# Optimization experiments

Hardware: AMD Instinct MI355X
Metric: run time of the kernel (lower is better)

The kernel has to match this reference:

```python
import jax, jax.numpy as jnp
import numpy as np
import math

IMG_COUNT = 5      # total_length = id_length + 1
NUM_TOKENS = 576   # (768//32)**2, the is_1024_resolution branch
CHANNELS = 1280
N_SEL = 288        # sa32 * NUM_TOKENS
HEADS = 20


def setup_inputs() -> dict:
    key = jax.random.key(0)
    ks = jax.random.split(key, 7)
    hidden_states = jax.random.normal(ks[0], (2 * IMG_COUNT, NUM_TOKENS, CHANNELS), dtype=jnp.float32)
    scale = 0.02
    Wq = jax.random.normal(ks[1], (CHANNELS, CHANNELS), dtype=jnp.float32) * scale
    Wk = jax.random.normal(ks[2], (CHANNELS, CHANNELS), dtype=jnp.float32) * scale
    Wv = jax.random.normal(ks[3], (CHANNELS, CHANNELS), dtype=jnp.float32) * scale
    Wo = jax.random.normal(ks[4], (CHANNELS, CHANNELS), dtype=jnp.float32) * scale
    bo = jnp.zeros((CHANNELS,), dtype=jnp.float32)
    # per-image random spatial token subsets (cal_attn_indice_xl_effcient_memory)
    indices = jax.random.randint(ks[5], (IMG_COUNT, N_SEL), 0, NUM_TOKENS, dtype=jnp.int64)
    return {"hidden_states": hidden_states, "Wq": Wq, "Wk": Wk, "Wv": Wv,
            "Wo": Wo, "bo": bo, "indices": indices, "heads": HEADS}


def _sdpa_block(q_in, kv_in, Wq, Wk, Wv, Wo, bo, heads):
    """Faithful __call2__: linear q/k/v, multi-head SDPA, output projection."""
    B, Tq, C = q_in.shape
    Tk = kv_in.shape[1]
    hd = C // heads
    q = (q_in @ Wq.T).reshape(B, Tq, heads, hd).transpose(0, 2, 1, 3)   # [B,H,Tq,hd]
    k = (kv_in @ Wk.T).reshape(B, Tk, heads, hd).transpose(0, 2, 1, 3)  # [B,H,Tk,hd]
    v = (kv_in @ Wv.T).reshape(B, Tk, heads, hd).transpose(0, 2, 1, 3)
    scale = 1.0 / math.sqrt(hd)
    scores = jnp.einsum('bhqd,bhkd->bhqk', q, k) * scale
    probs = jax.nn.softmax(scores, axis=-1)
    o = jnp.einsum('bhqk,bhkd->bhqd', probs, v)
    o = o.transpose(0, 2, 1, 3).reshape(B, Tq, C)
    return o @ Wo.T + bo


def reference(hidden_states, Wq, Wk, Wv, Wo, bo, indices, heads):
    B, T, C = hidden_states.shape
    P = indices.shape[0]          # img_count
    hs = hidden_states.reshape(2, P, T, C)
    # gathered[p] = hs[:, p, indices[p], :] -> [2, P, n_sel, C]
    gathered = hs[:, jnp.arange(P)[:, None], indices, :]
    outs = []
    for i in range(P):            # small fixed loop over images (structurally distinct KV banks)
        cur = hs[:, i]            # [2, T, C]
        others = jnp.concatenate([gathered[:, p] for p in range(P) if p != i], axis=1)
        enc = jnp.concatenate([others, cur], axis=1)  # [2, (P-1)*n_sel + T, C]
        outs.append(_sdpa_block(cur, enc, Wq, Wk, Wv, Wo, bo, heads))
    return jnp.stack(outs, axis=1).reshape(B, T, C)
```

## Files before the change

### kernel.cpp

```cpp
#include <hip/hip_runtime.h>

typedef __bf16 bf16_t;
typedef __attribute__((ext_vector_type(4))) __bf16 bf16x4;
typedef __attribute__((ext_vector_type(8))) __bf16 bf16x8;
typedef __attribute__((ext_vector_type(4))) float f32x4;

#define MFMA_BF16(a, b, c) __builtin_amdgcn_mfma_f32_16x16x32_bf16((a), (b), (c), 0, 0, 0)

namespace {

constexpr int PIMG  = 5;
constexpr int TTOK  = 576;
constexpr int CCH   = 1280;
constexpr int NSEL  = 288;
constexpr int NH    = 20;
constexpr int ROWS  = 2 * PIMG * TTOK;
constexpr int TKEYS = 4 * NSEL + TTOK;
constexpr int KT_TILES = TKEYS / 64;
constexpr size_t NXE = (size_t)ROWS * CCH;
constexpr size_t NWE = (size_t)CCH * CCH;

__device__ __forceinline__ bf16x8 cvt8(const float* p) {
  const float4 f0 = *(const float4*)p;
  const float4 f1 = *(const float4*)(p + 4);
  bf16x8 r;
  r[0] = (bf16_t)f0.x; r[1] = (bf16_t)f0.y; r[2] = (bf16_t)f0.z; r[3] = (bf16_t)f0.w;
  r[4] = (bf16_t)f1.x; r[5] = (bf16_t)f1.y; r[6] = (bf16_t)f1.z; r[7] = (bf16_t)f1.w;
  return r;
}

__global__ __launch_bounds__(256) void cvt_kernel(
    const float* __restrict__ X, const float* __restrict__ W0, const float* __restrict__ W1,
    const float* __restrict__ W2, const float* __restrict__ W3,
    bf16_t* __restrict__ Xb, bf16_t* __restrict__ Wb0, bf16_t* __restrict__ Wb1,
    bf16_t* __restrict__ Wb2, bf16_t* __restrict__ Wb3) {
  const int y = blockIdx.y;
  const float* src = y == 0 ? X : (y == 1 ? W0 : (y == 2 ? W1 : (y == 3 ? W2 : W3)));
  bf16_t* dst = y == 0 ? Xb : (y == 1 ? Wb0 : (y == 2 ? Wb1 : (y == 3 ? Wb2 : Wb3)));
  const size_t n = y == 0 ? NXE : NWE;
  const size_t idx = ((size_t)blockIdx.x * 256 + threadIdx.x) * 8;
  if (idx < n) *(bf16x8*)&dst[idx] = cvt8(&src[idx]);
}

template <bool BIAS, typename CT>
__device__ __forceinline__ void gemm_nt_body(const bf16_t* __restrict__ A,
                                             const bf16_t* __restrict__ B,
                                             const float* __restrict__ bias,
                                             CT* __restrict__ C,
                                             int bm, int bn, float scale) {
  constexpr int LDT = 72;
  __shared__ bf16_t As[128 * LDT];
  __shared__ bf16_t Bs[128 * LDT];

  const int tid  = threadIdx.x;
  const int lane = tid & 63;
  const int wave = tid >> 6;
  const int quad = lane >> 4;
  const int l16  = lane & 15;
  const int wr   = (wave >> 1) * 64;
  const int wc   = (wave & 1) * 64;
  const int m0   = bm * 128;
  const int n0   = bn * 128;
  const int srow = tid >> 3;
  const int scol = (tid & 7) * 8;

  bf16x8 pa[4], pb[4];
  auto loadAB = [&](int k0) {
#pragma unroll
    for (int p = 0; p < 4; ++p) {
      pa[p] = *(const bf16x8*)&A[(size_t)(m0 + srow + 32 * p) * CCH + k0 + scol];
      pb[p] = *(const bf16x8*)&B[(size_t)(n0 + srow + 32 * p) * CCH + k0 + scol];
    }
  };
  loadAB(0);

  f32x4 acc[4][4];
#pragma unroll
  for (int i = 0; i < 4; ++i)
#pragma unroll
    for (int j = 0; j < 4; ++j) acc[i][j] = (f32x4){0.f, 0.f, 0.f, 0.f};

  for (int it = 0; it < CCH / 64; ++it) {
#pragma unroll
    for (int p = 0; p < 4; ++p) {
      *(bf16x8*)&As[(srow + 32 * p) * LDT + scol] = pa[p];
      *(bf16x8*)&Bs[(srow + 32 * p) * LDT + scol] = pb[p];
    }
    __syncthreads();
    if (it < CCH / 64 - 1) loadAB((it + 1) * 64);
#pragma unroll
    for (int ks = 0; ks < 2; ++ks) {
      bf16x8 af[4], bfr[4];
#pragma unroll
      for (int i = 0; i < 4; ++i)
        af[i] = *(const bf16x8*)&As[(wr + 16 * i + l16) * LDT + ks * 32 + quad * 8];
#pragma unroll
      for (int j = 0; j < 4; ++j)
        bfr[j] = *(const bf16x8*)&Bs[(wc + 16 * j + l16) * LDT + ks * 32 + quad * 8];
#pragma unroll
      for (int i = 0; i < 4; ++i)
#pragma unroll
        for (int j = 0; j < 4; ++j)
          acc[i][j] = MFMA_BF16(af[i], bfr[j], acc[i][j]);
    }
    if (it < CCH / 64 - 1) __syncthreads();
  }

#pragma unroll
  for (int j = 0; j < 4; ++j) {
    const int col = n0 + wc + 16 * j + l16;
    const float bv = BIAS ? bias[col] : 0.f;
#pragma unroll
    for (int i = 0; i < 4; ++i) {
#pragma unroll
      for (int r = 0; r < 4; ++r) {
        const int row = m0 + wr + 16 * i + quad * 4 + r;
        const float val = acc[i][j][r] * scale + bv;
        if constexpr (sizeof(CT) == 2)
          C[(size_t)row * CCH + col] = (CT)val;
        else
          C[(size_t)row * CCH + col] = val;
      }
    }
  }
}

__global__ __launch_bounds__(256, 3) void qkv_gemm_kernel(
    const bf16_t* __restrict__ Xb,
    const bf16_t* __restrict__ Wqb, const bf16_t* __restrict__ Wkb, const bf16_t* __restrict__ Wvb,
    bf16_t* __restrict__ Qf, bf16_t* __restrict__ Kf, bf16_t* __restrict__ Vf) {
  const bf16_t* W = blockIdx.z == 0 ? Wqb : (blockIdx.z == 1 ? Wkb : Wvb);
  bf16_t* O = blockIdx.z == 0 ? Qf : (blockIdx.z == 1 ? Kf : Vf);
  const float scl = blockIdx.z == 0 ? 0.125f : 1.0f;
  gemm_nt_body<false, bf16_t>(Xb, W, nullptr, O, blockIdx.x, blockIdx.y, scl);
}

__global__ __launch_bounds__(256, 3) void out_gemm_kernel(
    const bf16_t* __restrict__ Of, const bf16_t* __restrict__ Wob,
    const float* __restrict__ bo, float* __restrict__ out) {
  gemm_nt_body<true, float>(Of, Wob, bo, out, blockIdx.x, blockIdx.y, 1.0f);
}

__global__ __launch_bounds__(128, 2) void attn_kernel(
    const bf16_t* __restrict__ Qf, const bf16_t* __restrict__ Kf, const bf16_t* __restrict__ Vf,
    const int* __restrict__ indices, bf16_t* __restrict__ Ofull) {
  __shared__ unsigned short kvrow[TKEYS];
  __shared__ __align__(16) bf16_t Vts[2][64 * 64];

  const int tid  = threadIdx.x;
  const int lane = tid & 63;
  const int wave = tid >> 6;
  const int quad = lane >> 4;
  const int l16  = lane & 15;

  const int b   = blockIdx.x;
  const int xcd = b & 7;
  const int t   = b >> 3;
  const int gi  = t / 9;
  const int qt  = t - gi * 9;
  const int g   = xcd + 8 * gi;
  const int h   = g % NH;
  const int si  = g / NH;
  const int s   = si / PIMG;
  const int ii  = si % PIMG;

  const int r0 = si * TTOK + qt * 64;
  const int hc = h * 64;

  bf16x8 aq[4][2];
#pragma unroll
  for (int n = 0; n < 4; ++n)
#pragma unroll
    for (int h2 = 0; h2 < 2; ++h2)
      aq[n][h2] = *(const bf16x8*)&Qf[(size_t)(r0 + 16 * n + l16) * CCH + hc + quad * 8 + 32 * h2];

  for (int j = tid; j < TKEYS; j += 128) {
    int row;
    if (j < 4 * NSEL) {
      const int jp = j / NSEL;
      const int jj = j - jp * NSEL;
      const int p  = jp + (jp >= ii ? 1 : 0);
      row = (s * PIMG + p) * TTOK + indices[p * NSEL + jj];
    } else {
      row = si * TTOK + (j - 4 * NSEL);
    }
    kvrow[j] = (unsigned short)row;
  }
  __syncthreads();

  const int kidx = 32 * wave + ((l16 >> 2) << 3) + (l16 & 3);

  const int va = tid >> 3;
  const int vc = (tid & 7) * 8;

  bf16x8 kq[2][2], kn[2][2], vs[4], vn[4];
#pragma unroll
  for (int kg = 0; kg < 2; ++kg) {
    const int krow = kvrow[kidx + 4 * kg];
    kq[kg][0] = *(const bf16x8*)&Kf[(size_t)krow * CCH + hc + quad * 8];
    kq[kg][1] = *(const bf16x8*)&Kf[(size_t)krow * CCH + hc + quad * 8 + 32];
  }
#pragma unroll
  for (int e = 0; e < 4; ++e)
    vs[e] = *(const bf16x8*)&Vf[(size_t)kvrow[4 * va + e] * CCH + hc + vc];

  float l_part[4] = {0.f, 0.f, 0.f, 0.f};
  f32x4 oacc[4][4];
#pragma unroll
  for (int n = 0; n < 4; ++n)
#pragma unroll
    for (int dg = 0; dg < 4; ++dg) oacc[n][dg] = (f32x4){0.f, 0.f, 0.f, 0.f};

  for (int kt = 0; kt < KT_TILES; ++kt) {
    {
      unsigned int* V32 = (unsigned int*)&Vts[kt & 1][0];
      const unsigned short* q0 = (const unsigned short*)&vs[0];
      const unsigned short* q1 = (const unsigned short*)&vs[1];
      const unsigned short* q2 = (const unsigned short*)&vs[2];
      const unsigned short* q3 = (const unsigned short*)&vs[3];
#pragma unroll
      for (int x = 0; x < 8; ++x) {
        const int sx = (vc >> 1) ^ (x << 2);
        V32[(vc + x) * 32 + ((2 * va) ^ sx)]     = (unsigned int)q0[x] | ((unsigned int)q1[x] << 16);
        V32[(vc + x) * 32 + ((2 * va + 1) ^ sx)] = (unsigned int)q2[x] | ((unsigned int)q3[x] << 16);
      }
    }

    if (kt + 1 < KT_TILES) {
      const int kb = (kt + 1) * 64;
#pragma unroll
      for (int kg = 0; kg < 2; ++kg) {
        const int krow = kvrow[kb + kidx + 4 * kg];
        kn[kg][0] = *(const bf16x8*)&Kf[(size_t)krow * CCH + hc + quad * 8];
        kn[kg][1] = *(const bf16x8*)&Kf[(size_t)krow * CCH + hc + quad * 8 + 32];
      }
#pragma unroll
      for (int e = 0; e < 4; ++e)
        vn[e] = *(const bf16x8*)&Vf[(size_t)kvrow[kb + 4 * va + e] * CCH + hc + vc];
    }

    bf16x8 pa[4];
#pragma unroll
    for (int kg = 0; kg < 2; ++kg) {
#pragma unroll
      for (int n = 0; n < 4; ++n) {
        f32x4 z = (f32x4){0.f, 0.f, 0.f, 0.f};
        z = MFMA_BF16(kq[kg][0], aq[n][0], z);
        z = MFMA_BF16(kq[kg][1], aq[n][1], z);
#pragma unroll
        for (int r = 0; r < 4; ++r) {
          const float pv = __expf(z[r]);
          l_part[n] += pv;
          pa[n][4 * kg + r] = (bf16_t)pv;
        }
      }
    }

    __syncthreads();

    const bf16_t* __restrict__ Vb = &Vts[kt & 1][0];
#pragma unroll
    for (int dg = 0; dg < 4; ++dg) {
      const int d  = 16 * dg + l16;
      const int sw = (d & 56) ^ ((d & 7) << 3);
      const bf16x8 vf = *(const bf16x8*)&Vb[d * 64 + ((32 * wave + 8 * quad) ^ sw)];
#pragma unroll
      for (int n = 0; n < 4; ++n)
        oacc[n][dg] = MFMA_BF16(pa[n], vf, oacc[n][dg]);
    }

#pragma unroll
    for (int kg = 0; kg < 2; ++kg) {
      kq[kg][0] = kn[kg][0];
      kq[kg][1] = kn[kg][1];
    }
#pragma unroll
    for (int e = 0; e < 4; ++e) vs[e] = vn[e];
  }

  __syncthreads();

  float* lred = (float*)kvrow;
  float* linv = lred + 512;
#pragma unroll
  for (int n = 0; n < 4; ++n)
    lred[(16 * n + l16) * 8 + 4 * wave + quad] = l_part[n];
  __syncthreads();
  if (tid < 64) {
    float tt = 0.f;
#pragma unroll
    for (int i = 0; i < 8; ++i) tt += lred[tid * 8 + i];
    linv[tid] = 1.f / tt;
  }
  __syncthreads();

  float* Osc = (float*)&Vts[0][0];
  if (wave == 0) {
#pragma unroll
    for (int n = 0; n < 4; ++n)
#pragma unroll
      for (int r = 0; r < 4; ++r) {
        const int q = 16 * n + 4 * quad + r;
#pragma unroll
        for (int dg = 0; dg < 4; ++dg)
          Osc[q * 64 + 16 * dg + l16] = oacc[n][dg][r];
      }
  }
  __syncthreads();
  if (wave == 1) {
#pragma unroll
    for (int n = 0; n < 4; ++n)
#pragma unroll
      for (int r = 0; r < 4; ++r) {
        const int q   = 16 * n + 4 * quad + r;
        const float inv = linv[q];
#pragma unroll
        for (int dg = 0; dg < 4; ++dg) {
          const float val = (Osc[q * 64 + 16 * dg + l16] + oacc[n][dg][r]) * inv;
          Ofull[(size_t)(r0 + q) * CCH + hc + 16 * dg + l16] = (bf16_t)val;
        }
      }
  }
}

}

extern "C" void kernel_launch(void* const* d_in, const int* in_sizes, int n_in,
                              void* d_out, int out_size, void* d_ws, size_t ws_size,
                              hipStream_t stream) {
  const float* hs = (const float*)d_in[0];
  const float* Wq = (const float*)d_in[1];
  const float* Wk = (const float*)d_in[2];
  const float* Wv = (const float*)d_in[3];
  const float* Wo = (const float*)d_in[4];
  const float* bo = (const float*)d_in[5];
  const int* indices = (const int*)d_in[6];
  float* out = (float*)d_out;

  bf16_t* Qf  = (bf16_t*)d_ws;
  bf16_t* Kf  = Qf + NXE;
  bf16_t* Vf  = Kf + NXE;
  bf16_t* Xb  = Vf + NXE;
  bf16_t* Of  = Xb;
  bf16_t* Wqb = Xb + NXE;
  bf16_t* Wkb = Wqb + NWE;
  bf16_t* Wvb = Wkb + NWE;
  bf16_t* Wob = Wvb + NWE;

  dim3 g0((NXE + 2047) / 2048, 5);
  cvt_kernel<<<g0, dim3(256), 0, stream>>>(hs, Wq, Wk, Wv, Wo, Xb, Wqb, Wkb, Wvb, Wob);

  dim3 g1(ROWS / 128, CCH / 128, 3);
  qkv_gemm_kernel<<<g1, dim3(256), 0, stream>>>(Xb, Wqb, Wkb, Wvb, Qf, Kf, Vf);

  attn_kernel<<<dim3(1800), dim3(128), 0, stream>>>(Qf, Kf, Vf, indices, Of);

  dim3 g3(ROWS / 128, CCH / 128, 1);
  out_gemm_kernel<<<g3, dim3(256), 0, stream>>>(Of, Wob, bo, out);
}
```

Baseline: 303.0 us.

## Load GEMM tiles directly into LDS with global_load_lds

Replaces the register-staged global-to-LDS copy in the projection GEMM with direct global_load_lds 16-byte transfers, and drops the padded LDS stride to a dense 64-wide layout. It aims to cut VGPR use and the extra LDS write instructions. In exchange it loses the register prefetch of the next k-tile, so loads are no longer overlapped with MFMA work. The unpadded layout may also cause LDS bank conflicts on the fragment reads.

```diff
diff --git a/kernel.cpp b/kernel.cpp
--- a/kernel.cpp
+++ b/kernel.cpp
@@ -27,6 +27,12 @@
   r[0] = (bf16_t)f0.x; r[1] = (bf16_t)f0.y; r[2] = (bf16_t)f0.z; r[3] = (bf16_t)f0.w;
   r[4] = (bf16_t)f1.x; r[5] = (bf16_t)f1.y; r[6] = (bf16_t)f1.z; r[7] = (bf16_t)f1.w;
   return r;
+}
+
+__device__ __forceinline__ void gld_lds16(const bf16_t* g, bf16_t* l) {
+  __builtin_amdgcn_global_load_lds(
+      (const __attribute__((address_space(1))) unsigned int*)g,
+      (__attribute__((address_space(3))) unsigned int*)l, 16, 0, 0);
 }
 
 __global__ __launch_bounds__(256) void cvt_kernel(
@@ -48,9 +54,8 @@
                                              const float* __restrict__ bias,
                                              CT* __restrict__ C,
                                              int bm, int bn, float scale) {
-  constexpr int LDT = 72;
-  __shared__ bf16_t As[128 * LDT];
-  __shared__ bf16_t Bs[128 * LDT];
+  __shared__ bf16_t As[128 * 64];
+  __shared__ bf16_t Bs[128 * 64];
 
   const int tid  = threadIdx.x;
   const int lane = tid & 63;
@@ -61,18 +66,9 @@
   const int wc   = (wave & 1) * 64;
   const int m0   = bm * 128;
   const int n0   = bn * 128;
-  const int srow = tid >> 3;
-  const int scol = (tid & 7) * 8;
-
-  bf16x8 pa[4], pb[4];
-  auto loadAB = [&](int k0) {
-#pragma unroll
-    for (int p = 0; p < 4; ++p) {
-      pa[p] = *(const bf16x8*)&A[(size_t)(m0 + srow + 32 * p) * CCH + k0 + scol];
-      pb[p] = *(const bf16x8*)&B[(size_t)(n0 + srow + 32 * p) * CCH + k0 + scol];
-    }
-  };
-  loadAB(0);
+
+  const int srow = (lane >> 3);
+  const int scol = (lane & 7) * 8;
 
   f32x4 acc[4][4];
 #pragma unroll
@@ -81,22 +77,23 @@
     for (int j = 0; j < 4; ++j) acc[i][j] = (f32x4){0.f, 0.f, 0.f, 0.f};
 
   for (int it = 0; it < CCH / 64; ++it) {
-#pragma unroll
-    for (int p = 0; p < 4; ++p) {
-      *(bf16x8*)&As[(srow + 32 * p) * LDT + scol] = pa[p];
-      *(bf16x8*)&Bs[(srow + 32 * p) * LDT + scol] = pb[p];
+    const int k0 = it * 64;
+#pragma unroll
+    for (int j = 0; j < 4; ++j) {
+      const int r = 32 * wave + 8 * j + srow;
+      gld_lds16(&A[(size_t)(m0 + r) * CCH + k0 + scol], &As[(32 * wave + 8 * j) * 64]);
+      gld_lds16(&B[(size_t)(n0 + r) * CCH + k0 + scol], &Bs[(32 * wave + 8 * j) * 64]);
     }
     __syncthreads();
-    if (it < CCH / 64 - 1) loadAB((it + 1) * 64);
 #pragma unroll
     for (int ks = 0; ks < 2; ++ks) {
       bf16x8 af[4], bfr[4];
 #pragma unroll
       for (int i = 0; i < 4; ++i)
-        af[i] = *(const bf16x8*)&As[(wr + 16 * i + l16) * LDT + ks * 32 + quad * 8];
+        af[i] = *(const bf16x8*)&As[(wr + 16 * i + l16) * 64 + ks * 32 + quad * 8];
 #pragma unroll
       for (int j = 0; j < 4; ++j)
-        bfr[j] = *(const bf16x8*)&Bs[(wc + 16 * j + l16) * LDT + ks * 32 + quad * 8];
+        bfr[j] = *(const bf16x8*)&Bs[(wc + 16 * j + l16) * 64 + ks * 32 + quad * 8];
 #pragma unroll
       for (int i = 0; i < 4; ++i)
 #pragma unroll
```

Result: slower. 310.6 us (+2.5%).
